# Kernel tuning notes

Hardware: AMD Instinct MI355X
Metric: run time of the kernel (lower is better)

Reference implementation:

```python
import jax, jax.numpy as jnp
import numpy as np

D_IN = 1024
D_OUT = 1024
NUM_HEAD = 16
HEAD_DIM = D_OUT // NUM_HEAD
CTX = 2048


def setup_inputs() -> dict:
    key = jax.random.key(0)
    ks = jax.random.split(key, 7)
    s = 0.02
    x = jax.random.normal(ks[0], (2, CTX, D_IN), dtype=jnp.float32)
    Wq = jax.random.normal(ks[1], (D_IN, D_OUT), dtype=jnp.float32) * s
    Wk = jax.random.normal(ks[2], (D_IN, D_OUT), dtype=jnp.float32) * s
    Wv = jax.random.normal(ks[3], (D_IN, D_OUT), dtype=jnp.float32) * s
    Wo = jax.random.normal(ks[4], (D_OUT, D_OUT), dtype=jnp.float32) * s
    bo = jax.random.normal(ks[5], (D_OUT,), dtype=jnp.float32) * s
    return {"x": x, "Wq": Wq, "Wk": Wk, "Wv": Wv, "Wo": Wo, "bo": bo}


def reference(x, Wq, Wk, Wv, Wo, bo):
    B, T, _ = x.shape
    # QKV projections, split into heads: [B, H, T, hd]
    def split_heads(y):
        return y.reshape(B, T, NUM_HEAD, HEAD_DIM).transpose(0, 2, 1, 3)
    q = split_heads(x @ Wq)
    k = split_heads(x @ Wk)
    v = split_heads(x @ Wv)
    # scaled causal attention scores [B, H, T, T]
    scores = jnp.einsum("bhqd,bhkd->bhqk", q, k) / jnp.sqrt(
        jnp.asarray(HEAD_DIM, dtype=x.dtype))
    causal = jnp.tril(jnp.ones((T, T), dtype=bool))  # mask buffer triu(diag=1) -> keep lower tri
    scores = jnp.where(causal[None, None], scores, jnp.asarray(-jnp.inf, dtype=x.dtype))
    attn = jax.nn.softmax(scores, axis=-1)
    # dropout with droprate=0.0 is identity
    ctx = jnp.einsum("bhqk,bhkd->bhqd", attn, v)
    ctx = ctx.transpose(0, 2, 1, 3).reshape(B, T, D_OUT)
    return ctx @ Wo + bo
```

## Files before the change

### kernel.cpp

```cpp
#include <hip/hip_runtime.h>

typedef __bf16 bf16x8 __attribute__((ext_vector_type(8)));
typedef float f32x4 __attribute__((ext_vector_type(4)));

__device__ inline float bf2f(unsigned short u) {
    unsigned int x = ((unsigned int)u) << 16;
    return __builtin_bit_cast(float, x);
}
__device__ inline unsigned short f2bf(float f) {
    unsigned int x = __builtin_bit_cast(unsigned int, f);
    x += 0x7fff + ((x >> 16) & 1);
    return (unsigned short)(x >> 16);
}

__device__ __forceinline__ void gl_lds16(const unsigned short* g, unsigned short* l)
{
    __builtin_amdgcn_global_load_lds(
        (const __attribute__((address_space(1))) void*)g,
        (__attribute__((address_space(3))) void*)l, 16, 0, 0);
}

__global__ __launch_bounds__(256)
void conv_bf16(const float* __restrict__ in, unsigned short* __restrict__ out)
{
    const size_t i = ((size_t)blockIdx.x * 256 + threadIdx.x) * 8;
    float4 a = *reinterpret_cast<const float4*>(in + i);
    float4 b = *reinterpret_cast<const float4*>(in + i + 4);
    unsigned short t[8] = { f2bf(a.x), f2bf(a.y), f2bf(a.z), f2bf(a.w),
                            f2bf(b.x), f2bf(b.y), f2bf(b.z), f2bf(b.w) };
    *reinterpret_cast<uint4*>(out + i) = *reinterpret_cast<uint4*>(t);
}

__global__ __launch_bounds__(256)
void wconv(const float* __restrict__ W0, const float* __restrict__ W1,
           const float* __restrict__ W2, unsigned short* __restrict__ wT)
{
    __shared__ unsigned short T[64][72];
    const int z = blockIdx.z;
    const float* W = (z == 0) ? W0 : (z == 1) ? W1 : W2;
    unsigned short* dstBase = wT + (size_t)z * 1024 * 1024;

    const int k0 = blockIdx.y * 64, n0 = blockIdx.x * 64;
    const int r = threadIdx.x >> 2, c0 = (threadIdx.x & 3) * 16;
    const float* src = W + (size_t)(k0 + r) * 1024 + n0 + c0;
    #pragma unroll
    for (int j = 0; j < 16; j += 4) {
        float4 f = *reinterpret_cast<const float4*>(src + j);
        T[r][c0 + j]     = f2bf(f.x);
        T[r][c0 + j + 1] = f2bf(f.y);
        T[r][c0 + j + 2] = f2bf(f.z);
        T[r][c0 + j + 3] = f2bf(f.w);
    }
    __syncthreads();
    unsigned short* dst = dstBase + (size_t)(n0 + r) * 1024 + k0 + c0;
    #pragma unroll
    for (int h = 0; h < 2; ++h) {
        unsigned short t8[8];
        #pragma unroll
        for (int j = 0; j < 8; ++j) t8[j] = T[c0 + h * 8 + j][r];
        *reinterpret_cast<uint4*>(dst + h * 8) = *reinterpret_cast<uint4*>(t8);
    }
}

template <int MODE>
__global__ __launch_bounds__(256)
void gemm128(const unsigned short* __restrict__ A,
             const unsigned short* __restrict__ BT,
             void* __restrict__ C0, void* __restrict__ C1,
             void* __restrict__ C2, const float* __restrict__ bias)
{
    __shared__ unsigned short As[128 * 32];
    __shared__ unsigned short Bs[128 * 32];

    const int tid = threadIdx.x;
    const int wave = tid >> 6, lane = tid & 63, quad = lane >> 4, l16 = lane & 15;
    const int wm = wave >> 1, wn = wave & 1;
    const int mBase = blockIdx.y * 128, nBase = blockIdx.x * 128;

    f32x4 acc[4][4] = {};

    const int srow = lane >> 2, sko = (lane & 3) * 8;

    for (int kb = 0; kb < 1024; kb += 32) {
        __syncthreads();
        #pragma unroll
        for (int j = 0; j < 2; ++j) {
            const int seg = wave * 2 + j;
            gl_lds16(A  + (size_t)(mBase + seg * 16 + srow) * 1024 + kb + sko,
                     As + seg * 512);
            gl_lds16(BT + (size_t)(nBase + seg * 16 + srow) * 1024 + kb + sko,
                     Bs + seg * 512);
        }
        __syncthreads();

        bf16x8 af[4], bf[4];
        #pragma unroll
        for (int t = 0; t < 4; ++t) {
            af[t] = *reinterpret_cast<const bf16x8*>(&As[(wm * 64 + t * 16 + l16) * 32 + quad * 8]);
            bf[t] = *reinterpret_cast<const bf16x8*>(&Bs[(wn * 64 + t * 16 + l16) * 32 + quad * 8]);
        }
        #pragma unroll
        for (int ti = 0; ti < 4; ++ti)
            #pragma unroll
            for (int tj = 0; tj < 4; ++tj)
                acc[ti][tj] = __builtin_amdgcn_mfma_f32_16x16x32_bf16(
                    af[ti], bf[tj], acc[ti][tj], 0, 0, 0);
    }

    #pragma unroll
    for (int ti = 0; ti < 4; ++ti) {
        const int row0 = mBase + wm * 64 + ti * 16 + quad * 4;
        #pragma unroll
        for (int tj = 0; tj < 4; ++tj) {
            const int col = nBase + wn * 64 + tj * 16 + l16;
            if constexpr (MODE == 0) {
                if (col < 1024) {
                    unsigned short* qb = (unsigned short*)C0;
                    #pragma unroll
                    for (int i = 0; i < 4; ++i)
                        qb[(size_t)(row0 + i) * 1024 + col] = f2bf(acc[ti][tj][i]);
                } else if (col < 2048) {
                    unsigned short* kb = (unsigned short*)C1;
                    #pragma unroll
                    for (int i = 0; i < 4; ++i)
                        kb[(size_t)(row0 + i) * 1024 + col - 1024] = f2bf(acc[ti][tj][i]);
                } else {
                    unsigned short* vT = (unsigned short*)C2;
                    unsigned short t4[4] = { f2bf(acc[ti][tj][0]), f2bf(acc[ti][tj][1]),
                                             f2bf(acc[ti][tj][2]), f2bf(acc[ti][tj][3]) };
                    *reinterpret_cast<uint2*>(&vT[(size_t)(col - 2048) * 4096 + row0]) =
                        *reinterpret_cast<uint2*>(t4);
                }
            } else {
                float* out = (float*)C0;
                const float ba = bias[col];
                #pragma unroll
                for (int i = 0; i < 4; ++i)
                    out[(size_t)(row0 + i) * 1024 + col] = acc[ti][tj][i] + ba;
            }
        }
    }
}

#define LDA 72

__global__ __launch_bounds__(256)
void attn2(const unsigned short* __restrict__ q,
           const unsigned short* __restrict__ k,
           const unsigned short* __restrict__ vT,
           unsigned short* __restrict__ ctx)
{
    __shared__ unsigned short Ks[64 * LDA];
    __shared__ unsigned short Vs[64 * LDA];
    __shared__ unsigned short Ps[64 * LDA];

    const int tid  = threadIdx.x;
    const int wave = tid >> 6, lane = tid & 63, quad = lane >> 4, l16 = lane & 15;
    const int qt = 31 - blockIdx.x;
    const int bh = blockIdx.y;
    const int b = bh >> 4, h = bh & 15;
    const int tRowBase = b * 2048;
    const int colBase  = h * 64;
    const int qBase    = qt * 64;

    bf16x8 aq[2];
    {
        const unsigned short* qrow =
            q + (size_t)(tRowBase + qBase + wave * 16 + l16) * 1024 + colBase;
        aq[0] = *reinterpret_cast<const bf16x8*>(qrow + quad * 8);
        aq[1] = *reinterpret_cast<const bf16x8*>(qrow + 32 + quad * 8);
    }

    f32x4 o[4] = {};
    float ls[4] = {};

    const int sr = tid >> 3, so = (tid & 7) * 8;

    uint4 kr0, kr1, vr0, vr1;
    {
        const size_t kg = (size_t)(tRowBase + sr) * 1024 + colBase + so;
        kr0 = *reinterpret_cast<const uint4*>(&k[kg]);
        kr1 = *reinterpret_cast<const uint4*>(&k[kg + (size_t)32 * 1024]);
        const size_t vg = (size_t)(colBase + sr) * 4096 + tRowBase + so;
        vr0 = *reinterpret_cast<const uint4*>(&vT[vg]);
        vr1 = *reinterpret_cast<const uint4*>(&vT[vg + (size_t)32 * 4096]);
    }

    const int nkt = qt + 1;
    for (int kt = 0; kt < nkt; ++kt) {
        __syncthreads();
        *reinterpret_cast<uint4*>(&Ks[sr * LDA + so])        = kr0;
        *reinterpret_cast<uint4*>(&Ks[(sr + 32) * LDA + so]) = kr1;
        *reinterpret_cast<uint4*>(&Vs[sr * LDA + so])        = vr0;
        *reinterpret_cast<uint4*>(&Vs[(sr + 32) * LDA + so]) = vr1;
        __syncthreads();

        if (kt + 1 < nkt) {
            const size_t kg = (size_t)(tRowBase + (kt + 1) * 64 + sr) * 1024 + colBase + so;
            kr0 = *reinterpret_cast<const uint4*>(&k[kg]);
            kr1 = *reinterpret_cast<const uint4*>(&k[kg + (size_t)32 * 1024]);
            const size_t vg = (size_t)(colBase + sr) * 4096 + tRowBase + (kt + 1) * 64 + so;
            vr0 = *reinterpret_cast<const uint4*>(&vT[vg]);
            vr1 = *reinterpret_cast<const uint4*>(&vT[vg + (size_t)32 * 4096]);
        }

        f32x4 sc[4] = {};
        #pragma unroll
        for (int t = 0; t < 4; ++t) {
            #pragma unroll
            for (int kf = 0; kf < 2; ++kf) {
                bf16x8 bk = *reinterpret_cast<const bf16x8*>(
                    &Ks[(t * 16 + l16) * LDA + kf * 32 + quad * 8]);
                sc[t] = __builtin_amdgcn_mfma_f32_16x16x32_bf16(aq[kf], bk, sc[t], 0, 0, 0);
            }
        }

        const bool diag = (kt == qt);
        #pragma unroll
        for (int t = 0; t < 4; ++t) {
            const int ki = kt * 64 + t * 16 + l16;
            #pragma unroll
            for (int r = 0; r < 4; ++r) {
                float p = __expf(sc[t][r] * 0.125f);
                if (diag) {
                    const int qi = qBase + wave * 16 + quad * 4 + r;
                    if (ki > qi) p = 0.0f;
                }
                ls[r] += p;
                Ps[(wave * 16 + quad * 4 + r) * LDA + t * 16 + l16] = f2bf(p);
            }
        }

        bf16x8 ap0 = *reinterpret_cast<const bf16x8*>(&Ps[(wave * 16 + l16) * LDA + quad * 8]);
        bf16x8 ap1 = *reinterpret_cast<const bf16x8*>(&Ps[(wave * 16 + l16) * LDA + 32 + quad * 8]);
        #pragma unroll
        for (int t = 0; t < 4; ++t) {
            #pragma unroll
            for (int kf = 0; kf < 2; ++kf) {
                bf16x8 bv = *reinterpret_cast<const bf16x8*>(
                    &Vs[(t * 16 + l16) * LDA + kf * 32 + quad * 8]);
                o[t] = __builtin_amdgcn_mfma_f32_16x16x32_bf16(kf ? ap1 : ap0, bv, o[t], 0, 0, 0);
            }
        }
    }

    #pragma unroll
    for (int off = 1; off < 16; off <<= 1)
        #pragma unroll
        for (int r = 0; r < 4; ++r)
            ls[r] += __shfl_xor(ls[r], off);

    #pragma unroll
    for (int r = 0; r < 4; ++r) {
        const float inv = 1.0f / ls[r];
        const size_t gr = (size_t)(tRowBase + qBase + wave * 16 + quad * 4 + r) * 1024 + colBase;
        #pragma unroll
        for (int t = 0; t < 4; ++t)
            ctx[gr + t * 16 + l16] = f2bf(o[t][r] * inv);
    }
}

extern "C" void kernel_launch(void* const* d_in, const int* in_sizes, int n_in,
                              void* d_out, int out_size, void* d_ws, size_t ws_size,
                              hipStream_t stream)
{
    const float* x  = (const float*)d_in[0];
    const float* Wq = (const float*)d_in[1];
    const float* Wk = (const float*)d_in[2];
    const float* Wv = (const float*)d_in[3];
    const float* Wo = (const float*)d_in[4];
    const float* bo = (const float*)d_in[5];
    float* out = (float*)d_out;

    unsigned short* xb     = (unsigned short*)d_ws;
    unsigned short* qb     = xb + (size_t)4096 * 1024;
    unsigned short* kb     = qb + (size_t)4096 * 1024;
    unsigned short* vT     = kb + (size_t)4096 * 1024;
    unsigned short* ctx    = xb;
    unsigned short* wqkvT  = (unsigned short*)d_out;
    unsigned short* woT    = qb;

    conv_bf16<<<2048, 256, 0, stream>>>(x, xb);

    wconv<<<dim3(16, 16, 3), 256, 0, stream>>>(Wq, Wk, Wv, wqkvT);

    gemm128<0><<<dim3(24, 32), 256, 0, stream>>>(xb, wqkvT, qb, kb, vT, nullptr);

    attn2<<<dim3(32, 32), 256, 0, stream>>>(qb, kb, vT, ctx);

    wconv<<<dim3(16, 16, 1), 256, 0, stream>>>(Wo, Wo, Wo, woT);

    gemm128<2><<<dim3(8, 32), 256, 0, stream>>>(ctx, woT, out, nullptr, nullptr, bo);
}
```

Baseline: 211.5 us.

## Use 128-key tiles in attention with causal fragment skipping; fuse prep kernels

Each attention iteration now processes 128 keys instead of 64, halving the loop trip count and barrier pairs. Within the last tile it skips 16-key score fragments and P·V k-slices that lie entirely above the causal diagonal, zero-padding odd fragment counts. The x conversion and QKV weight transposition are merged into one launch, and Wo's bf16 copy moves to the k buffer. The larger tiles raise LDS use and register pressure (more prefetch registers), which may reduce occupancy.

```diff
diff --git a/kernel.cpp b/kernel.cpp
--- a/kernel.cpp
+++ b/kernel.cpp
@@ -21,26 +21,25 @@
 }
 
 __global__ __launch_bounds__(256)
-void conv_bf16(const float* __restrict__ in, unsigned short* __restrict__ out)
-{
-    const size_t i = ((size_t)blockIdx.x * 256 + threadIdx.x) * 8;
-    float4 a = *reinterpret_cast<const float4*>(in + i);
-    float4 b = *reinterpret_cast<const float4*>(in + i + 4);
-    unsigned short t[8] = { f2bf(a.x), f2bf(a.y), f2bf(a.z), f2bf(a.w),
-                            f2bf(b.x), f2bf(b.y), f2bf(b.z), f2bf(b.w) };
-    *reinterpret_cast<uint4*>(out + i) = *reinterpret_cast<uint4*>(t);
-}
-
-__global__ __launch_bounds__(256)
-void wconv(const float* __restrict__ W0, const float* __restrict__ W1,
-           const float* __restrict__ W2, unsigned short* __restrict__ wT)
+void prep(const float* __restrict__ x, unsigned short* __restrict__ xb,
+          const float* __restrict__ Wq, const float* __restrict__ Wk,
+          const float* __restrict__ Wv, unsigned short* __restrict__ wT)
 {
     __shared__ unsigned short T[64][72];
-    const int z = blockIdx.z;
-    const float* W = (z == 0) ? W0 : (z == 1) ? W1 : W2;
+    if (blockIdx.x < 2048) {
+        const size_t i = ((size_t)blockIdx.x * 256 + threadIdx.x) * 8;
+        float4 a = *reinterpret_cast<const float4*>(x + i);
+        float4 b = *reinterpret_cast<const float4*>(x + i + 4);
+        unsigned short t[8] = { f2bf(a.x), f2bf(a.y), f2bf(a.z), f2bf(a.w),
+                                f2bf(b.x), f2bf(b.y), f2bf(b.z), f2bf(b.w) };
+        *reinterpret_cast<uint4*>(xb + i) = *reinterpret_cast<uint4*>(t);
+        return;
+    }
+    const int blk = blockIdx.x - 2048;
+    const int z = blk >> 8, within = blk & 255;
+    const float* W = (z == 0) ? Wq : (z == 1) ? Wk : Wv;
     unsigned short* dstBase = wT + (size_t)z * 1024 * 1024;
-
-    const int k0 = blockIdx.y * 64, n0 = blockIdx.x * 64;
+    const int k0 = (within >> 4) * 64, n0 = (within & 15) * 64;
     const int r = threadIdx.x >> 2, c0 = (threadIdx.x & 3) * 16;
     const float* src = W + (size_t)(k0 + r) * 1024 + n0 + c0;
     #pragma unroll
@@ -53,6 +52,32 @@
     }
     __syncthreads();
     unsigned short* dst = dstBase + (size_t)(n0 + r) * 1024 + k0 + c0;
+    #pragma unroll
+    for (int h = 0; h < 2; ++h) {
+        unsigned short t8[8];
+        #pragma unroll
+        for (int j = 0; j < 8; ++j) t8[j] = T[c0 + h * 8 + j][r];
+        *reinterpret_cast<uint4*>(dst + h * 8) = *reinterpret_cast<uint4*>(t8);
+    }
+}
+
+__global__ __launch_bounds__(256)
+void wconv(const float* __restrict__ W, unsigned short* __restrict__ wT)
+{
+    __shared__ unsigned short T[64][72];
+    const int k0 = blockIdx.y * 64, n0 = blockIdx.x * 64;
+    const int r = threadIdx.x >> 2, c0 = (threadIdx.x & 3) * 16;
+    const float* src = W + (size_t)(k0 + r) * 1024 + n0 + c0;
+    #pragma unroll
+    for (int j = 0; j < 16; j += 4) {
+        float4 f = *reinterpret_cast<const float4*>(src + j);
+        T[r][c0 + j]     = f2bf(f.x);
+        T[r][c0 + j + 1] = f2bf(f.y);
+        T[r][c0 + j + 2] = f2bf(f.z);
+        T[r][c0 + j + 3] = f2bf(f.w);
+    }
+    __syncthreads();
+    unsigned short* dst = wT + (size_t)(n0 + r) * 1024 + k0 + c0;
     #pragma unroll
     for (int h = 0; h < 2; ++h) {
         unsigned short t8[8];
@@ -142,17 +167,18 @@
     }
 }
 
-#define LDA 72
+#define LDK 72
+#define LDV 136
 
 __global__ __launch_bounds__(256)
-void attn2(const unsigned short* __restrict__ q,
+void attn3(const unsigned short* __restrict__ q,
            const unsigned short* __restrict__ k,
            const unsigned short* __restrict__ vT,
            unsigned short* __restrict__ ctx)
 {
-    __shared__ unsigned short Ks[64 * LDA];
-    __shared__ unsigned short Vs[64 * LDA];
-    __shared__ unsigned short Ps[64 * LDA];
+    __shared__ unsigned short Ks[128 * LDK];
+    __shared__ unsigned short Vs[64 * LDV];
+    __shared__ unsigned short Ps[64 * LDV];
 
     const int tid  = threadIdx.x;
     const int wave = tid >> 6, lane = tid & 63, quad = lane >> 4, l16 = lane & 15;
@@ -174,72 +200,85 @@
     f32x4 o[4] = {};
     float ls[4] = {};
 
-    const int sr = tid >> 3, so = (tid & 7) * 8;
-
-    uint4 kr0, kr1, vr0, vr1;
+    const int skr = tid >> 3, sko = (tid & 7) * 8;
+    const int svr = tid >> 4, svc = (tid & 15) * 8;
+
+    uint4 kr[4], vr[4];
     {
-        const size_t kg = (size_t)(tRowBase + sr) * 1024 + colBase + so;
-        kr0 = *reinterpret_cast<const uint4*>(&k[kg]);
-        kr1 = *reinterpret_cast<const uint4*>(&k[kg + (size_t)32 * 1024]);
-        const size_t vg = (size_t)(colBase + sr) * 4096 + tRowBase + so;
-        vr0 = *reinterpret_cast<const uint4*>(&vT[vg]);
-        vr1 = *reinterpret_cast<const uint4*>(&vT[vg + (size_t)32 * 4096]);
-    }
-
-    const int nkt = qt + 1;
+        const size_t kg = (size_t)(tRowBase + skr) * 1024 + colBase + sko;
+        #pragma unroll
+        for (int m = 0; m < 4; ++m)
+            kr[m] = *reinterpret_cast<const uint4*>(&k[kg + (size_t)m * 32 * 1024]);
+        const size_t vg = (size_t)(colBase + svr) * 4096 + tRowBase + svc;
+        #pragma unroll
+        for (int m = 0; m < 4; ++m)
+            vr[m] = *reinterpret_cast<const uint4*>(&vT[vg + (size_t)m * 16 * 4096]);
+    }
+
+    const int nkt = (qt + 2) >> 1;
     for (int kt = 0; kt < nkt; ++kt) {
         __syncthreads();
-        *reinterpret_cast<uint4*>(&Ks[sr * LDA + so])        = kr0;
-        *reinterpret_cast<uint4*>(&Ks[(sr + 32) * LDA + so]) = kr1;
-        *reinterpret_cast<uint4*>(&Vs[sr * LDA + so])        = vr0;
-        *reinterpret_cast<uint4*>(&Vs[(sr + 32) * LDA + so]) = vr1;
+        #pragma unroll
+        for (int m = 0; m < 4; ++m) {
+            *reinterpret_cast<uint4*>(&Ks[(skr + 32 * m) * LDK + sko]) = kr[m];
+            *reinterpret_cast<uint4*>(&Vs[(svr + 16 * m) * LDV + svc]) = vr[m];
+        }
         __syncthreads();
 
         if (kt + 1 < nkt) {
-            const size_t kg = (size_t)(tRowBase + (kt + 1) * 64 + sr) * 1024 + colBase + so;
-            kr0 = *reinterpret_cast<const uint4*>(&k[kg]);
-            kr1 = *reinterpret_cast<const uint4*>(&k[kg + (size_t)32 * 1024]);
-            const size_t vg = (size_t)(colBase + sr) * 4096 + tRowBase + (kt + 1) * 64 + so;
-            vr0 = *reinterpret_cast<const uint4*>(&vT[vg]);
-            vr1 = *reinterpret_cast<const uint4*>(&vT[vg + (size_t)32 * 4096]);
-        }
-
-        f32x4 sc[4] = {};
-        #pragma unroll
-        for (int t = 0; t < 4; ++t) {
+            const size_t kg = (size_t)(tRowBase + (kt + 1) * 128 + skr) * 1024 + colBase + sko;
+            #pragma unroll
+            for (int m = 0; m < 4; ++m)
+                kr[m] = *reinterpret_cast<const uint4*>(&k[kg + (size_t)m * 32 * 1024]);
+            const size_t vg = (size_t)(colBase + svr) * 4096 + tRowBase + (kt + 1) * 128 + svc;
+            #pragma unroll
+            for (int m = 0; m < 4; ++m)
+                vr[m] = *reinterpret_cast<const uint4*>(&vT[vg + (size_t)m * 16 * 4096]);
+        }
+
+        const int kLim = qBase + 63 - kt * 128;
+        const int nf = (kLim >= 127) ? 8 : ((kLim >> 4) + 1);
+        const bool lastT = (kt == nkt - 1);
+
+        #pragma unroll
+        for (int t = 0; t < 8; ++t) {
+            if (t >= nf) continue;
+            f32x4 sc = {};
             #pragma unroll
             for (int kf = 0; kf < 2; ++kf) {
                 bf16x8 bk = *reinterpret_cast<const bf16x8*>(
-                    &Ks[(t * 16 + l16) * LDA + kf * 32 + quad * 8]);
-                sc[t] = __builtin_amdgcn_mfma_f32_16x16x32_bf16(aq[kf], bk, sc[t], 0, 0, 0);
+                    &Ks[(t * 16 + l16) * LDK + kf * 32 + quad * 8]);
+                sc = __builtin_amdgcn_mfma_f32_16x16x32_bf16(aq[kf], bk, sc, 0, 0, 0);
             }
-        }
-
-        const bool diag = (kt == qt);
-        #pragma unroll
-        for (int t = 0; t < 4; ++t) {
-            const int ki = kt * 64 + t * 16 + l16;
+            const int ki = kt * 128 + t * 16 + l16;
             #pragma unroll
             for (int r = 0; r < 4; ++r) {
-                float p = __expf(sc[t][r] * 0.125f);
-                if (diag) {
+                float p = __expf(sc[r] * 0.125f);
+                if (lastT) {
                     const int qi = qBase + wave * 16 + quad * 4 + r;
                     if (ki > qi) p = 0.0f;
                 }
                 ls[r] += p;
-                Ps[(wave * 16 + quad * 4 + r) * LDA + t * 16 + l16] = f2bf(p);
+                Ps[(wave * 16 + quad * 4 + r) * LDV + t * 16 + l16] = f2bf(p);
             }
         }
-
-        bf16x8 ap0 = *reinterpret_cast<const bf16x8*>(&Ps[(wave * 16 + l16) * LDA + quad * 8]);
-        bf16x8 ap1 = *reinterpret_cast<const bf16x8*>(&Ps[(wave * 16 + l16) * LDA + 32 + quad * 8]);
-        #pragma unroll
-        for (int t = 0; t < 4; ++t) {
-            #pragma unroll
-            for (int kf = 0; kf < 2; ++kf) {
+        if (nf & 1) {
+            #pragma unroll
+            for (int r = 0; r < 4; ++r)
+                Ps[(wave * 16 + quad * 4 + r) * LDV + nf * 16 + l16] = 0;
+        }
+
+        const int nkf = (nf + 1) >> 1;
+        #pragma unroll
+        for (int kf = 0; kf < 4; ++kf) {
+            if (kf >= nkf) continue;
+            bf16x8 ap = *reinterpret_cast<const bf16x8*>(
+                &Ps[(wave * 16 + l16) * LDV + kf * 32 + quad * 8]);
+            #pragma unroll
+            for (int t = 0; t < 4; ++t) {
                 bf16x8 bv = *reinterpret_cast<const bf16x8*>(
-                    &Vs[(t * 16 + l16) * LDA + kf * 32 + quad * 8]);
-                o[t] = __builtin_amdgcn_mfma_f32_16x16x32_bf16(kf ? ap1 : ap0, bv, o[t], 0, 0, 0);
+                    &Vs[(t * 16 + l16) * LDV + kf * 32 + quad * 8]);
+                o[t] = __builtin_amdgcn_mfma_f32_16x16x32_bf16(ap, bv, o[t], 0, 0, 0);
             }
         }
     }
@@ -278,17 +317,15 @@
     unsigned short* vT     = kb + (size_t)4096 * 1024;
     unsigned short* ctx    = xb;
     unsigned short* wqkvT  = (unsigned short*)d_out;
-    unsigned short* woT    = qb;
-
-    conv_bf16<<<2048, 256, 0, stream>>>(x, xb);
-
-    wconv<<<dim3(16, 16, 3), 256, 0, stream>>>(Wq, Wk, Wv, wqkvT);
+    unsigned short* woT    = kb;
+
+    prep<<<2816, 256, 0, stream>>>(x, xb, Wq, Wk, Wv, wqkvT);
 
     gemm128<0><<<dim3(24, 32), 256, 0, stream>>>(xb, wqkvT, qb, kb, vT, nullptr);
 
-    attn2<<<dim3(32, 32), 256, 0, stream>>>(qb, kb, vT, ctx);
-
-    wconv<<<dim3(16, 16, 1), 256, 0, stream>>>(Wo, Wo, Wo, woT);
+    attn3<<<dim3(32, 32), 256, 0, stream>>>(qb, kb, vT, ctx);
+
+    wconv<<<dim3(16, 16), 256, 0, stream>>>(Wo, woT);
 
     gemm128<2><<<dim3(8, 32), 256, 0, stream>>>(ctx, woT, out, nullptr, nullptr, bo);
 }
```

After: 310.9 us. 1.47x slower.
